# Optimization experiments

Hardware: AMD Instinct MI355X
Metric: run time of the kernel (lower is better)

Reference implementation:

```python
import jax, jax.numpy as jnp
import numpy as np

CUTOFF = 5.0
B, A, N, G, F = 32, 256, 64, 50, 128


def _ssp(v):
    # shifted softplus used by SchNet filter network
    return jax.nn.softplus(v) - jnp.log(2.0).astype(v.dtype)


def setup_inputs() -> dict:
    key = jax.random.key(0)
    ks = jax.random.split(key, 8)
    x = jax.random.normal(ks[0], (B, A, F), dtype=jnp.float32)
    r_ij = jax.random.uniform(ks[1], (B, A, N), dtype=jnp.float32) * 4.5
    f_ij = jax.random.normal(ks[2], (B, A, N, G), dtype=jnp.float32)
    pairwise_mask = jnp.ones((B, A, N), dtype=jnp.float32)
    neighbors = jax.random.randint(ks[3], (B, A, N), 0, A, dtype=jnp.int64)
    in2f_w = jax.random.normal(ks[4], (F, F), dtype=jnp.float32) / np.sqrt(F)
    fw1 = jax.random.normal(ks[5], (G, F), dtype=jnp.float32) / np.sqrt(G)
    fb1 = jnp.zeros((F,), dtype=jnp.float32)
    fw2 = jax.random.normal(ks[6], (F, F), dtype=jnp.float32) / np.sqrt(F)
    fb2 = jnp.zeros((F,), dtype=jnp.float32)
    return {"x": x, "r_ij": r_ij, "f_ij": f_ij, "pairwise_mask": pairwise_mask,
            "neighbors": neighbors, "in2f_w": in2f_w, "fw1": fw1, "fb1": fb1,
            "fw2": fw2, "fb2": fb2}


def reference(x, r_ij, f_ij, pairwise_mask, neighbors, in2f_w, fw1, fb1, fw2, fb2):
    # filter network: Dense(G->F, shifted softplus) -> Dense(F->F, linear)
    W = _ssp(jnp.einsum('bang,gf->banf', f_ij, fw1) + fb1)
    W = jnp.einsum('banh,hf->banf', W, fw2) + fb2          # (B,A,N,F)
    # cosine cutoff
    C = 0.5 * (jnp.cos(r_ij * (jnp.pi / CUTOFF)) + 1.0)
    C = C * (r_ij < CUTOFF).astype(r_ij.dtype)
    W = W * C[..., None]
    # in2f dense (no bias)
    y = jnp.einsum('bai,if->baf', x, in2f_w)               # (B,A,F)
    # gather neighbor features along atom axis
    b_idx = jnp.arange(B)[:, None, None]
    y_nbh = y[b_idx, neighbors]                             # (B,A,N,F)
    # elementwise filter multiply + masked sum over neighbor axis
    out = jnp.sum(y_nbh * W * pairwise_mask[..., None], axis=2)  # (B,A,F)
    return out
```

## Files before the change

### kernel.cpp

```cpp
#include <hip/hip_runtime.h>
#include <hip/hip_bf16.h>
#include <math.h>

#define Bdim 32
#define Adim 256
#define Ndim 64
#define Gdim 50
#define Fdim 128

typedef __attribute__((ext_vector_type(8)))  short short8;
typedef __attribute__((ext_vector_type(16))) float floatx16;

__device__ __forceinline__ unsigned short f2bf_u(float x) {
    __hip_bfloat16 h = __float2bfloat16(x);
    return __builtin_bit_cast(unsigned short, h);
}
__device__ __forceinline__ unsigned pk2bf(float a, float b) {
    return (unsigned)f2bf_u(a) | ((unsigned)f2bf_u(b) << 16);
}
__device__ __forceinline__ float bf2f(unsigned short v) {
    return __builtin_bit_cast(float, ((unsigned)v) << 16);
}
__device__ __forceinline__ float sspf(float v) {
    float t = __expf(-fabsf(v));
    return fmaxf(v, 0.0f) + __logf(1.0f + t) - 0.69314718056f;
}
__device__ __forceinline__ short8 mk8(unsigned a, unsigned b, unsigned c, unsigned d) {
    union { unsigned u[4]; short8 s; } t;
    t.u[0] = a; t.u[1] = b; t.u[2] = c; t.u[3] = d;
    return t.s;
}

__global__ __launch_bounds__(256) void in2f_mfma2(const float* __restrict__ x,
                                                  const float* __restrict__ w,
                                                  unsigned short* __restrict__ y) {
    __shared__ short sWT[128 * 132];
    __shared__ short sX [128 * 132];
    const int tid = threadIdx.x;

#pragma unroll 4
    for (int k = 0; k < 32; ++k) {
        int idx = tid + k * 256;
        float2 v = *(const float2*)(w + 2 * idx);
        int i = idx >> 6;
        int f = (2 * idx) & 127;
        sWT[f * 132 + i]       = (short)f2bf_u(v.x);
        sWT[(f + 1) * 132 + i] = (short)f2bf_u(v.y);
    }
    const float* xb = x + (size_t)blockIdx.x * (128 * 128);
#pragma unroll 4
    for (int k = 0; k < 32; ++k) {
        int idx = tid + k * 256;
        float2 v = *(const float2*)(xb + 2 * idx);
        int row = idx >> 6;
        int i = (2 * idx) & 127;
        *(unsigned*)&sX[row * 132 + i] = pk2bf(v.x, v.y);
    }
    __syncthreads();

    const int wv = tid >> 6, lane = tid & 63, lm = lane & 31, lh = lane >> 5;
    floatx16 acc[4];
#pragma unroll
    for (int jt = 0; jt < 4; ++jt)
#pragma unroll
        for (int e = 0; e < 16; ++e) acc[jt][e] = 0.0f;

#pragma unroll
    for (int ks = 0; ks < 8; ++ks) {
        int g0 = ks * 16 + lh * 8;
        const short* ap = &sX[(wv * 32 + lm) * 132 + g0];
        uint2 a0 = *(const uint2*)ap;
        uint2 a1 = *(const uint2*)(ap + 4);
        short8 a = mk8(a0.x, a0.y, a1.x, a1.y);
#pragma unroll
        for (int jt = 0; jt < 4; ++jt) {
            const short* bp = &sWT[(jt * 32 + lm) * 132 + g0];
            uint2 b0 = *(const uint2*)bp;
            uint2 b1 = *(const uint2*)(bp + 4);
            acc[jt] = __builtin_amdgcn_mfma_f32_32x32x16_bf16(
                a, mk8(b0.x, b0.y, b1.x, b1.y), acc[jt], 0, 0, 0);
        }
    }
    const int rbase = blockIdx.x * 128 + wv * 32;
#pragma unroll
    for (int jt = 0; jt < 4; ++jt)
#pragma unroll
        for (int r = 0; r < 16; ++r) {
            int row = rbase + (r & 3) + 8 * (r >> 2) + 4 * lh;
            y[(size_t)row * 128 + jt * 32 + lm] = f2bf_u(acc[jt][r]);
        }
}

#define SF1 68
#define SF2 132
#define SFI 60

__global__ __launch_bounds__(256, 2) void cfconv_mfma3(
    const float* __restrict__ r_ij, const float* __restrict__ f_ij,
    const float* __restrict__ mask, const int* __restrict__ nbr,
    const float* __restrict__ fw1, const float* __restrict__ fb1,
    const float* __restrict__ fw2, const float* __restrict__ fb2,
    const unsigned short* __restrict__ ybf, float* __restrict__ out)
{
    __shared__ short sFw1[128 * SF1];
    __shared__ short sFw2[128 * SF2];
    __shared__ short sFij[128 * SFI + 16];
    __shared__ float sCm[128];
    __shared__ int   sNbr[128];
    __shared__ float sRed[4 * 128];

    const int tid = threadIdx.x, wv = tid >> 6, lane = tid & 63;
    const int lm = lane & 31, lh = lane >> 5;

    for (int idx = tid; idx < Gdim * 128; idx += 256) {
        int g = idx >> 7, f = idx & 127;
        sFw1[f * SF1 + g] = (short)f2bf_u(fw1[idx]);
    }
    for (int idx = tid; idx < 128 * 14; idx += 256) {
        int f = idx / 14, g = Gdim + idx % 14;
        sFw1[f * SF1 + g] = (g == Gdim) ? (short)f2bf_u(fb1[f]) : (short)0;
    }
    for (int idx = tid; idx < 128 * 128; idx += 256) {
        int h = idx >> 7, f = idx & 127;
        sFw2[f * SF2 + h] = (short)f2bf_u(fw2[idx]);
    }
    for (int idx = tid; idx < 128 * 5; idx += 256) {
        int row = idx / 5, k = idx - row * 5;
        *(unsigned*)&sFij[row * SFI + 50 + 2 * k] = (k == 0) ? 0x00003F80u : 0u;
    }
    if (tid < 8) *(unsigned*)&sFij[128 * SFI + 2 * tid] = 0u;

    float fb2v[4];
#pragma unroll
    for (int jt = 0; jt < 4; ++jt) fb2v[jt] = fb2[jt * 32 + lm];

    for (int it = 0; it < 4; ++it) {
        const int sp = blockIdx.x + 1024 * it;

        const float* fp = f_ij + (size_t)sp * (2 * Ndim * Gdim);
#pragma unroll
        for (int k = 0; k < 13; ++k) {
            int idx = tid + k * 256;
            if (idx < 3200) {
                float2 v = *(const float2*)(fp + 2 * idx);
                int row = idx / 25;
                int g   = 2 * idx - row * 50;
                *(unsigned*)&sFij[row * SFI + g] = pk2bf(v.x, v.y);
            }
        }
        if (tid < 128) {
            int site = sp * 2 + (tid >> 6), n = tid & 63;
            float r = r_ij[(size_t)site * Ndim + n];
            float c = 0.5f * (__cosf(r * 0.62831853071796f) + 1.0f);
            c = (r < 5.0f) ? c : 0.0f;
            sCm[tid]  = c * mask[(size_t)site * Ndim + n];
            sNbr[tid] = nbr[(size_t)site * Ndim + n];
        }
        __syncthreads();

        const int rowb = wv * 32;
        unsigned A2[8][4];
#pragma unroll
        for (int ft = 0; ft < 4; ++ft) {
            floatx16 a1;
#pragma unroll
            for (int e = 0; e < 16; ++e) a1[e] = 0.0f;
#pragma unroll
            for (int ks = 0; ks < 4; ++ks) {
                int g0 = ks * 16 + lh * 8;
                const short* ap = &sFw1[(ft * 32 + lm) * SF1 + g0];
                uint2 a0 = *(const uint2*)ap;
                uint2 a1v = *(const uint2*)(ap + 4);
                const short* bp = &sFij[(rowb + lm) * SFI + g0];
                uint2 b0 = *(const uint2*)bp;
                uint2 b1v = *(const uint2*)(bp + 4);
                a1 = __builtin_amdgcn_mfma_f32_32x32x16_bf16(
                    mk8(a0.x, a0.y, a1v.x, a1v.y),
                    mk8(b0.x, b0.y, b1v.x, b1v.y), a1, 0, 0, 0);
            }
            unsigned P[8], X[8];
#pragma unroll
            for (int q = 0; q < 8; ++q)
                P[q] = pk2bf(sspf(a1[2 * q]), sspf(a1[2 * q + 1]));
#pragma unroll
            for (int q = 0; q < 8; ++q) X[q] = (unsigned)__shfl_xor((int)P[q], 32);
            A2[2*ft][0]   = lh ? X[2] : P[0];  A2[2*ft][1]   = lh ? X[3] : P[1];
            A2[2*ft][2]   = lh ? P[2] : X[0];  A2[2*ft][3]   = lh ? P[3] : X[1];
            A2[2*ft+1][0] = lh ? X[6] : P[4];  A2[2*ft+1][1] = lh ? X[7] : P[5];
            A2[2*ft+1][2] = lh ? P[6] : X[4];  A2[2*ft+1][3] = lh ? P[7] : X[5];
        }

        floatx16 acc2[4];
#pragma unroll
        for (int jt = 0; jt < 4; ++jt)
#pragma unroll
            for (int e = 0; e < 16; ++e) acc2[jt][e] = 0.0f;
#pragma unroll
        for (int ks = 0; ks < 8; ++ks) {
            short8 a = mk8(A2[ks][0], A2[ks][1], A2[ks][2], A2[ks][3]);
#pragma unroll
            for (int jt = 0; jt < 4; ++jt) {
                const short* bp = &sFw2[(jt * 32 + lm) * SF2 + ks * 16 + lh * 8];
                uint2 b0 = *(const uint2*)bp;
                uint2 b1 = *(const uint2*)(bp + 4);
                acc2[jt] = __builtin_amdgcn_mfma_f32_32x32x16_bf16(
                    a, mk8(b0.x, b0.y, b1.x, b1.y), acc2[jt], 0, 0, 0);
            }
        }

        const int ps = sp * 2 + (wv >> 1);
        float cmv[16]; int nbv[16];
#pragma unroll
        for (int rq = 0; rq < 4; ++rq) {
            float4 c4 = *(const float4*)&sCm[wv * 32 + rq * 8 + lh * 4];
            int4   n4 = *(const int4*)&sNbr[wv * 32 + rq * 8 + lh * 4];
            cmv[rq*4+0] = c4.x; cmv[rq*4+1] = c4.y; cmv[rq*4+2] = c4.z; cmv[rq*4+3] = c4.w;
            nbv[rq*4+0] = n4.x; nbv[rq*4+1] = n4.y; nbv[rq*4+2] = n4.z; nbv[rq*4+3] = n4.w;
        }
        const int bofs = (ps >> 8) * Adim;
        float part[4] = {0.f, 0.f, 0.f, 0.f};
#pragma unroll
        for (int r = 0; r < 16; ++r) {
            float cm = cmv[r];
            const unsigned short* yr = ybf + (size_t)(bofs + nbv[r]) * 128;
#pragma unroll
            for (int jt = 0; jt < 4; ++jt) {
                float yv = bf2f(yr[jt * 32 + lm]);
                part[jt] += (acc2[jt][r] + fb2v[jt]) * cm * yv;
            }
        }
#pragma unroll
        for (int jt = 0; jt < 4; ++jt) {
            float s = part[jt] + __shfl_xor(part[jt], 32);
            if (lh == 0) sRed[wv * 128 + jt * 32 + lm] = s;
        }
        __syncthreads();
        {
            int s = tid >> 7, f = tid & 127;
            out[(size_t)(sp * 2 + s) * 128 + f] =
                sRed[(2 * s) * 128 + f] + sRed[(2 * s + 1) * 128 + f];
        }
    }
}

extern "C" void kernel_launch(void* const* d_in, const int* in_sizes, int n_in,
                              void* d_out, int out_size, void* d_ws, size_t ws_size,
                              hipStream_t stream) {
    const float* x      = (const float*)d_in[0];
    const float* r_ij   = (const float*)d_in[1];
    const float* f_ij   = (const float*)d_in[2];
    const float* mask   = (const float*)d_in[3];
    const int*   nbr    = (const int*)d_in[4];
    const float* in2f_w = (const float*)d_in[5];
    const float* fw1    = (const float*)d_in[6];
    const float* fb1    = (const float*)d_in[7];
    const float* fw2    = (const float*)d_in[8];
    const float* fb2    = (const float*)d_in[9];
    float* out = (float*)d_out;
    unsigned short* y = (unsigned short*)d_ws;

    in2f_mfma2<<<64, 256, 0, stream>>>(x, in2f_w, y);
    cfconv_mfma3<<<1024, 256, 0, stream>>>(r_ij, f_ij, mask, nbr,
                                           fw1, fb1, fw2, fb2, y, out);
}
```

Before: 253.1 us.

## Register-prefetch f_ij fragments, swizzle fw2 LDS, raise occupancy to three blocks

The main kernel now loads each wave's f_ij fragments straight from global memory into registers in MFMA B-operand layout. The next site pair is prefetched while the current one computes, so the LDS staging buffer and the first barrier are gone. The fw2 shared tile uses an XOR swizzle instead of padding, and the cutoff, mask and neighbor loads move into registers per wave. The grid grows to 1536 blocks with launch bounds of 3, each block handling up to three site pairs. The prefetch registers raise register pressure, and the load imbalance across blocks (some do 2 pairs, some 3) may offset the gains.

New measurement: 240.7 us. 4.9% less time.

```diff
diff --git a/kernel.cpp b/kernel.cpp
--- a/kernel.cpp
+++ b/kernel.cpp
@@ -92,10 +92,148 @@
 }
 
 #define SF1 68
-#define SF2 132
-#define SFI 60
-
-__global__ __launch_bounds__(256, 2) void cfconv_mfma3(
+#define NSP 4096
+#define GRID2 1536
+
+struct FijRegs { float2 p[13]; };
+
+__device__ __forceinline__ FijRegs load_fij(const float* __restrict__ f_ij,
+                                            int sp, int row, int lh) {
+    FijRegs F;
+    const float* base = f_ij + (size_t)sp * (2 * Ndim * Gdim) + row * Gdim;
+#pragma unroll
+    for (int ks = 0; ks < 3; ++ks) {
+        int g0 = 16 * ks + 8 * lh;
+#pragma unroll
+        for (int j = 0; j < 4; ++j)
+            F.p[ks * 4 + j] = *(const float2*)(base + g0 + 2 * j);
+    }
+    F.p[12] = *(const float2*)(base + 48);
+    return F;
+}
+
+__device__ __forceinline__ void cf_body(
+    int sp, int par, const FijRegs& F, int nsp, FijRegs& Fn,
+    const float* __restrict__ f_ij, const float* __restrict__ r_ij,
+    const float* __restrict__ mask, const int* __restrict__ nbr,
+    const unsigned short* __restrict__ ybf, float* __restrict__ out,
+    float4 fb2v, const short* sFw1, const short* sFw2,
+    float (*sRed)[2][128], int wv, int lm, int lh, int row)
+{
+    short8 bfr[4];
+#pragma unroll
+    for (int ks = 0; ks < 3; ++ks)
+        bfr[ks] = mk8(pk2bf(F.p[ks*4+0].x, F.p[ks*4+0].y),
+                      pk2bf(F.p[ks*4+1].x, F.p[ks*4+1].y),
+                      pk2bf(F.p[ks*4+2].x, F.p[ks*4+2].y),
+                      pk2bf(F.p[ks*4+3].x, F.p[ks*4+3].y));
+    {
+        unsigned u0 = lh ? 0u : pk2bf(F.p[12].x, F.p[12].y);
+        unsigned u1 = lh ? 0u : 0x00003F80u;
+        bfr[3] = mk8(u0, u1, 0u, 0u);
+    }
+    if (nsp >= 0) Fn = load_fij(f_ij, nsp, row, lh);
+
+    unsigned A2[8][4];
+#pragma unroll
+    for (int ft = 0; ft < 4; ++ft) {
+        floatx16 a1;
+#pragma unroll
+        for (int e = 0; e < 16; ++e) a1[e] = 0.0f;
+#pragma unroll
+        for (int ks = 0; ks < 4; ++ks) {
+            const short* ap = &sFw1[(ft * 32 + lm) * SF1 + ks * 16 + lh * 8];
+            uint2 a0 = *(const uint2*)ap;
+            uint2 a1v = *(const uint2*)(ap + 4);
+            a1 = __builtin_amdgcn_mfma_f32_32x32x16_bf16(
+                mk8(a0.x, a0.y, a1v.x, a1v.y), bfr[ks], a1, 0, 0, 0);
+        }
+        unsigned P[8], X[8];
+#pragma unroll
+        for (int q = 0; q < 8; ++q)
+            P[q] = pk2bf(sspf(a1[2 * q]), sspf(a1[2 * q + 1]));
+#pragma unroll
+        for (int q = 0; q < 8; ++q) X[q] = (unsigned)__shfl_xor((int)P[q], 32);
+        A2[2*ft][0]   = lh ? X[2] : P[0];  A2[2*ft][1]   = lh ? X[3] : P[1];
+        A2[2*ft][2]   = lh ? P[2] : X[0];  A2[2*ft][3]   = lh ? P[3] : X[1];
+        A2[2*ft+1][0] = lh ? X[6] : P[4];  A2[2*ft+1][1] = lh ? X[7] : P[5];
+        A2[2*ft+1][2] = lh ? P[6] : X[4];  A2[2*ft+1][3] = lh ? P[7] : X[5];
+    }
+
+    floatx16 acc2[4];
+#pragma unroll
+    for (int jt = 0; jt < 4; ++jt)
+#pragma unroll
+        for (int e = 0; e < 16; ++e) acc2[jt][e] = 0.0f;
+#pragma unroll
+    for (int ks = 0; ks < 8; ++ks) {
+        short8 a = mk8(A2[ks][0], A2[ks][1], A2[ks][2], A2[ks][3]);
+#pragma unroll
+        for (int jt = 0; jt < 4; ++jt) {
+            int rw = jt * 32 + lm;
+            const short* bp = &sFw2[rw * 128 + ((ks * 16 + lh * 8) ^ ((rw & 15) << 3))];
+            uint2 b0 = *(const uint2*)bp;
+            uint2 b1 = *(const uint2*)(bp + 4);
+            acc2[jt] = __builtin_amdgcn_mfma_f32_32x32x16_bf16(
+                a, mk8(b0.x, b0.y, b1.x, b1.y), acc2[jt], 0, 0, 0);
+        }
+    }
+
+    const int site = sp * 2 + (wv >> 1);
+    float cmv[16]; int nbv[16];
+#pragma unroll
+    for (int rq = 0; rq < 4; ++rq) {
+        int off = site * Ndim + (wv & 1) * 32 + rq * 8 + lh * 4;
+        float4 r4 = *(const float4*)(r_ij + off);
+        float4 m4 = *(const float4*)(mask + off);
+        int4   n4 = *(const int4*)(nbr + off);
+        float rr[4] = { r4.x, r4.y, r4.z, r4.w };
+        float mm[4] = { m4.x, m4.y, m4.z, m4.w };
+        int   nn[4] = { n4.x, n4.y, n4.z, n4.w };
+#pragma unroll
+        for (int j = 0; j < 4; ++j) {
+            float c = 0.5f * (__cosf(rr[j] * 0.62831853071796f) + 1.0f);
+            c = (rr[j] < 5.0f) ? c : 0.0f;
+            cmv[rq * 4 + j] = c * mm[j];
+            nbv[rq * 4 + j] = nn[j];
+        }
+    }
+
+    const int bofs = (site >> 8) * Adim;
+    float part[4] = {0.f, 0.f, 0.f, 0.f};
+#pragma unroll
+    for (int r = 0; r < 16; ++r) {
+        float cm = cmv[r];
+        const unsigned short* yr = ybf + (size_t)(bofs + nbv[r]) * Fdim;
+#pragma unroll
+        for (int jt = 0; jt < 4; ++jt) {
+            float fb2j = (jt == 0) ? fb2v.x : (jt == 1) ? fb2v.y
+                       : (jt == 2) ? fb2v.z : fb2v.w;
+            float yv = bf2f(yr[jt * 32 + lm]);
+            part[jt] += (acc2[jt][r] + fb2j) * cm * yv;
+        }
+    }
+#pragma unroll
+    for (int jt = 0; jt < 4; ++jt) part[jt] += __shfl_xor(part[jt], 32);
+
+    const int s = wv >> 1;
+    if (wv & 1) {
+#pragma unroll
+        for (int k = 0; k < 2; ++k)
+            sRed[par][s][(2 * lh + k) * 32 + lm] = part[2 * lh + k];
+    }
+    __syncthreads();
+    if (!(wv & 1)) {
+#pragma unroll
+        for (int k = 0; k < 2; ++k) {
+            int jt = 2 * lh + k;
+            int f = jt * 32 + lm;
+            out[(size_t)site * Fdim + f] = part[jt] + sRed[par][s][f];
+        }
+    }
+}
+
+__global__ __launch_bounds__(256, 3) void cfconv_mfma4(
     const float* __restrict__ r_ij, const float* __restrict__ f_ij,
     const float* __restrict__ mask, const int* __restrict__ nbr,
     const float* __restrict__ fw1, const float* __restrict__ fb1,
@@ -103,14 +241,15 @@
     const unsigned short* __restrict__ ybf, float* __restrict__ out)
 {
     __shared__ short sFw1[128 * SF1];
-    __shared__ short sFw2[128 * SF2];
-    __shared__ short sFij[128 * SFI + 16];
-    __shared__ float sCm[128];
-    __shared__ int   sNbr[128];
-    __shared__ float sRed[4 * 128];
+    __shared__ short sFw2[128 * 128];
+    __shared__ float sRed[2][2][128];
 
     const int tid = threadIdx.x, wv = tid >> 6, lane = tid & 63;
     const int lm = lane & 31, lh = lane >> 5;
+    const int bid = blockIdx.x;
+    const int row = wv * 32 + lm;
+
+    FijRegs FA = load_fij(f_ij, bid, row, lh);
 
     for (int idx = tid; idx < Gdim * 128; idx += 256) {
         int g = idx >> 7, f = idx & 127;
@@ -122,125 +261,21 @@
     }
     for (int idx = tid; idx < 128 * 128; idx += 256) {
         int h = idx >> 7, f = idx & 127;
-        sFw2[f * SF2 + h] = (short)f2bf_u(fw2[idx]);
-    }
-    for (int idx = tid; idx < 128 * 5; idx += 256) {
-        int row = idx / 5, k = idx - row * 5;
-        *(unsigned*)&sFij[row * SFI + 50 + 2 * k] = (k == 0) ? 0x00003F80u : 0u;
-    }
-    if (tid < 8) *(unsigned*)&sFij[128 * SFI + 2 * tid] = 0u;
-
-    float fb2v[4];
-#pragma unroll
-    for (int jt = 0; jt < 4; ++jt) fb2v[jt] = fb2[jt * 32 + lm];
-
-    for (int it = 0; it < 4; ++it) {
-        const int sp = blockIdx.x + 1024 * it;
-
-        const float* fp = f_ij + (size_t)sp * (2 * Ndim * Gdim);
-#pragma unroll
-        for (int k = 0; k < 13; ++k) {
-            int idx = tid + k * 256;
-            if (idx < 3200) {
-                float2 v = *(const float2*)(fp + 2 * idx);
-                int row = idx / 25;
-                int g   = 2 * idx - row * 50;
-                *(unsigned*)&sFij[row * SFI + g] = pk2bf(v.x, v.y);
-            }
-        }
-        if (tid < 128) {
-            int site = sp * 2 + (tid >> 6), n = tid & 63;
-            float r = r_ij[(size_t)site * Ndim + n];
-            float c = 0.5f * (__cosf(r * 0.62831853071796f) + 1.0f);
-            c = (r < 5.0f) ? c : 0.0f;
-            sCm[tid]  = c * mask[(size_t)site * Ndim + n];
-            sNbr[tid] = nbr[(size_t)site * Ndim + n];
-        }
-        __syncthreads();
-
-        const int rowb = wv * 32;
-        unsigned A2[8][4];
-#pragma unroll
-        for (int ft = 0; ft < 4; ++ft) {
-            floatx16 a1;
-#pragma unroll
-            for (int e = 0; e < 16; ++e) a1[e] = 0.0f;
-#pragma unroll
-            for (int ks = 0; ks < 4; ++ks) {
-                int g0 = ks * 16 + lh * 8;
-                const short* ap = &sFw1[(ft * 32 + lm) * SF1 + g0];
-                uint2 a0 = *(const uint2*)ap;
-                uint2 a1v = *(const uint2*)(ap + 4);
-                const short* bp = &sFij[(rowb + lm) * SFI + g0];
-                uint2 b0 = *(const uint2*)bp;
-                uint2 b1v = *(const uint2*)(bp + 4);
-                a1 = __builtin_amdgcn_mfma_f32_32x32x16_bf16(
-                    mk8(a0.x, a0.y, a1v.x, a1v.y),
-                    mk8(b0.x, b0.y, b1v.x, b1v.y), a1, 0, 0, 0);
-            }
-            unsigned P[8], X[8];
-#pragma unroll
-            for (int q = 0; q < 8; ++q)
-                P[q] = pk2bf(sspf(a1[2 * q]), sspf(a1[2 * q + 1]));
-#pragma unroll
-            for (int q = 0; q < 8; ++q) X[q] = (unsigned)__shfl_xor((int)P[q], 32);
-            A2[2*ft][0]   = lh ? X[2] : P[0];  A2[2*ft][1]   = lh ? X[3] : P[1];
-            A2[2*ft][2]   = lh ? P[2] : X[0];  A2[2*ft][3]   = lh ? P[3] : X[1];
-            A2[2*ft+1][0] = lh ? X[6] : P[4];  A2[2*ft+1][1] = lh ? X[7] : P[5];
-            A2[2*ft+1][2] = lh ? P[6] : X[4];  A2[2*ft+1][3] = lh ? P[7] : X[5];
-        }
-
-        floatx16 acc2[4];
-#pragma unroll
-        for (int jt = 0; jt < 4; ++jt)
-#pragma unroll
-            for (int e = 0; e < 16; ++e) acc2[jt][e] = 0.0f;
-#pragma unroll
-        for (int ks = 0; ks < 8; ++ks) {
-            short8 a = mk8(A2[ks][0], A2[ks][1], A2[ks][2], A2[ks][3]);
-#pragma unroll
-            for (int jt = 0; jt < 4; ++jt) {
-                const short* bp = &sFw2[(jt * 32 + lm) * SF2 + ks * 16 + lh * 8];
-                uint2 b0 = *(const uint2*)bp;
-                uint2 b1 = *(const uint2*)(bp + 4);
-                acc2[jt] = __builtin_amdgcn_mfma_f32_32x32x16_bf16(
-                    a, mk8(b0.x, b0.y, b1.x, b1.y), acc2[jt], 0, 0, 0);
-            }
-        }
-
-        const int ps = sp * 2 + (wv >> 1);
-        float cmv[16]; int nbv[16];
-#pragma unroll
-        for (int rq = 0; rq < 4; ++rq) {
-            float4 c4 = *(const float4*)&sCm[wv * 32 + rq * 8 + lh * 4];
-            int4   n4 = *(const int4*)&sNbr[wv * 32 + rq * 8 + lh * 4];
-            cmv[rq*4+0] = c4.x; cmv[rq*4+1] = c4.y; cmv[rq*4+2] = c4.z; cmv[rq*4+3] = c4.w;
-            nbv[rq*4+0] = n4.x; nbv[rq*4+1] = n4.y; nbv[rq*4+2] = n4.z; nbv[rq*4+3] = n4.w;
-        }
-        const int bofs = (ps >> 8) * Adim;
-        float part[4] = {0.f, 0.f, 0.f, 0.f};
-#pragma unroll
-        for (int r = 0; r < 16; ++r) {
-            float cm = cmv[r];
-            const unsigned short* yr = ybf + (size_t)(bofs + nbv[r]) * 128;
-#pragma unroll
-            for (int jt = 0; jt < 4; ++jt) {
-                float yv = bf2f(yr[jt * 32 + lm]);
-                part[jt] += (acc2[jt][r] + fb2v[jt]) * cm * yv;
-            }
-        }
-#pragma unroll
-        for (int jt = 0; jt < 4; ++jt) {
-            float s = part[jt] + __shfl_xor(part[jt], 32);
-            if (lh == 0) sRed[wv * 128 + jt * 32 + lm] = s;
-        }
-        __syncthreads();
-        {
-            int s = tid >> 7, f = tid & 127;
-            out[(size_t)(sp * 2 + s) * 128 + f] =
-                sRed[(2 * s) * 128 + f] + sRed[(2 * s + 1) * 128 + f];
-        }
-    }
+        sFw2[f * 128 + (h ^ ((f & 15) << 3))] = (short)f2bf_u(fw2[idx]);
+    }
+    float4 fb2v;
+    fb2v.x = fb2[lm]; fb2v.y = fb2[32 + lm]; fb2v.z = fb2[64 + lm]; fb2v.w = fb2[96 + lm];
+    __syncthreads();
+
+    const int sp1 = bid + GRID2, sp2 = bid + 2 * GRID2;
+    FijRegs FB;
+    cf_body(bid, 0, FA, sp1, FB, f_ij, r_ij, mask, nbr, ybf, out,
+            fb2v, sFw1, sFw2, sRed, wv, lm, lh, row);
+    cf_body(sp1, 1, FB, (sp2 < NSP) ? sp2 : -1, FA, f_ij, r_ij, mask, nbr, ybf, out,
+            fb2v, sFw1, sFw2, sRed, wv, lm, lh, row);
+    if (sp2 < NSP)
+        cf_body(sp2, 0, FA, -1, FB, f_ij, r_ij, mask, nbr, ybf, out,
+                fb2v, sFw1, sFw2, sRed, wv, lm, lh, row);
 }
 
 extern "C" void kernel_launch(void* const* d_in, const int* in_sizes, int n_in,
@@ -260,6 +295,6 @@
     unsigned short* y = (unsigned short*)d_ws;
 
     in2f_mfma2<<<64, 256, 0, stream>>>(x, in2f_w, y);
-    cfconv_mfma3<<<1024, 256, 0, stream>>>(r_ij, f_ij, mask, nbr,
-                                           fw1, fb1, fw2, fb2, y, out);
-}
+    cfconv_mfma4<<<GRID2, 256, 0, stream>>>(r_ij, f_ij, mask, nbr,
+                                            fw1, fb1, fw2, fb2, y, out);
+}
```
